# Optimization experiments

Measured on AMD Instinct MI355X. Metric: run time of the kernel, lower is better.

## Reference

```python
import jax, jax.numpy as jnp
import numpy as np
from functools import partial

C = 96
D_STATE = 16
D_CONV = 4
EXPAND = 2
D_INNER = EXPAND * C
DT_RANK = (C + 15) // 16  # ceil(96/16) = 6
EPS = 1e-6


def _ln_cf(x, w, b):
    # channels_first LayerNorm over axis=1 of [B,C,D,H,W]
    u = jnp.mean(x, axis=1, keepdims=True)
    s = jnp.mean((x - u) ** 2, axis=1, keepdims=True)
    xn = (x - u) / jnp.sqrt(s + EPS)
    return w[None, :, None, None, None] * xn + b[None, :, None, None, None]


def _ln_last(x, w, b):
    u = jnp.mean(x, axis=-1, keepdims=True)
    s = jnp.mean((x - u) ** 2, axis=-1, keepdims=True)
    return (x - u) / jnp.sqrt(s + 1e-5) * w + b


def _mamba(x, Win, conv_w, conv_b, Wx, Wdt, bdt, A_log, Dp, Wout):
    # x: [B, L, C]
    B, L, _ = x.shape
    xz = jnp.einsum('blc,ec->ble', x, Win)           # [B,L,2*di]
    xin, z = xz[..., :D_INNER], xz[..., D_INNER:]
    # depthwise causal conv along L
    xt = jnp.transpose(xin, (0, 2, 1))               # [B,di,L]
    xt = jnp.pad(xt, ((0, 0), (0, 0), (D_CONV - 1, 0)))
    xc = jax.lax.conv_general_dilated(
        xt, conv_w[:, None, :], window_strides=(1,), padding='VALID',
        feature_group_count=D_INNER, dimension_numbers=('NCH', 'OIH', 'NCH'))
    xc = jax.nn.silu(xc + conv_b[None, :, None])
    xc = jnp.transpose(xc, (0, 2, 1))                # [B,L,di]
    x_dbl = jnp.einsum('bld,ed->ble', xc, Wx)        # [B,L,dt_rank+2*ds]
    dt_r = x_dbl[..., :DT_RANK]
    Bm = x_dbl[..., DT_RANK:DT_RANK + D_STATE]       # [B,L,ds]
    Cm = x_dbl[..., DT_RANK + D_STATE:]              # [B,L,ds]
    dt = jax.nn.softplus(jnp.einsum('blr,dr->bld', dt_r, Wdt) + bdt)
    A = -jnp.exp(A_log)                              # [di,ds]
    dA = jnp.exp(dt[..., None] * A)                  # [B,L,di,ds]
    dBx = (dt * xc)[..., None] * Bm[:, :, None, :]   # [B,L,di,ds]

    def comb(e1, e2):
        a1, b1 = e1
        a2, b2 = e2
        return a1 * a2, a2 * b1 + b2

    _, h = jax.lax.associative_scan(comb, (dA, dBx), axis=1)
    y = jnp.einsum('blds,bls->bld', h, Cm) + xc * Dp
    y = y * jax.nn.silu(z)
    return jnp.einsum('bld,cd->blc', y, Wout)


def setup_inputs() -> dict:
    key = jax.random.key(0)
    ks = jax.random.split(key, 16)
    g = lambda k, sh: jax.random.normal(k, sh, dtype=jnp.float32) * 0.02
    inp = {
        'x': jax.random.normal(ks[0], (2, C, 20, 20, 20), dtype=jnp.float32),
        'ln_w': jnp.ones((C,), jnp.float32), 'ln_b': jnp.zeros((C,), jnp.float32),
        'mln_w': jnp.ones((C,), jnp.float32), 'mln_b': jnp.zeros((C,), jnp.float32),
        'Win': g(ks[1], (2 * D_INNER, C)),
        'conv_w': g(ks[2], (D_INNER, D_CONV)), 'conv_b': jnp.zeros((D_INNER,), jnp.float32),
        'Wx': g(ks[3], (DT_RANK + 2 * D_STATE, D_INNER)),
        'Wdt': g(ks[4], (D_INNER, DT_RANK)), 'bdt': g(ks[5], (D_INNER,)),
        'A_log': jnp.log(jnp.broadcast_to(jnp.arange(1, D_STATE + 1, dtype=jnp.float32), (D_INNER, D_STATE))),
        'Dp': jnp.ones((D_INNER,), jnp.float32),
        'Wout': g(ks[6], (C, D_INNER)),
        'proj_w': g(ks[7], (C, 3 * C)), 'proj_b': jnp.zeros((C,), jnp.float32),
        'fc1_w': g(ks[8], (4 * C, C)), 'fc1_b': jnp.zeros((4 * C,), jnp.float32),
        'fc2_w': g(ks[9], (C, 4 * C)), 'fc2_b': jnp.zeros((C,), jnp.float32),
    }
    return inp


def reference(x, ln_w, ln_b, mln_w, mln_b, Win, conv_w, conv_b, Wx, Wdt, bdt,
              A_log, Dp, Wout, proj_w, proj_b, fc1_w, fc1_b, fc2_w, fc2_b):
    B, Cc, Dd, Hh, Ww = x.shape
    L = Dd * Hh * Ww
    x1 = _ln_cf(x, ln_w, ln_b)
    # three directional flattenings (cube, so reshape shapes match)
    outs = []
    for perm in ((0, 1, 2, 3, 4), (0, 1, 3, 4, 2), (0, 1, 4, 2, 3)):
        xp = jnp.transpose(x1, perm)                     # [B,C,a,b,c]
        xf = jnp.transpose(xp.reshape(B, Cc, L), (0, 2, 1))  # [B,L,C]
        xf = _ln_last(xf, mln_w, mln_b)
        y = _mamba(xf, Win, conv_w, conv_b, Wx, Wdt, bdt, A_log, Dp, Wout)
        outs.append(jnp.transpose(y, (0, 2, 1)).reshape(B, Cc, Dd, Hh, Ww))
    cat = jnp.concatenate(outs, axis=1)                  # [B,3C,D,H,W]
    out1 = jnp.einsum('oc,bcdhw->bodhw', proj_w, cat) + proj_b[None, :, None, None, None]
    out_res = x + out1
    h = _ln_cf(out_res, ln_w, ln_b)
    h = jnp.einsum('oc,bcdhw->bodhw', fc1_w, h) + fc1_b[None, :, None, None, None]
    h = jax.nn.gelu(h, approximate=False)
    h = jnp.einsum('oc,bcdhw->bodhw', fc2_w, h) + fc2_b[None, :, None, None, None]
    return h + out_res
```

## Files before the change

kernel.cpp:

```cpp
#include <hip/hip_runtime.h>
#include <math.h>

#define S   8000
#define BB  2
#define CC  96
#define DI  192
#define NS  16
#define RK  6
#define GG  6
#define NC  200
#define LC  40
#define ND  38

typedef __attribute__((ext_vector_type(8))) short bf16x8;
typedef __attribute__((ext_vector_type(4))) float f32x4;
typedef __attribute__((ext_vector_type(2))) float f32x2;

__device__ __forceinline__ int pos_from_l(int dir, int l) {
  if (dir == 0) return l;
  int a  = l / 400;
  int r  = l - a * 400;
  int bq = r / 20;
  int cq = r - bq * 20;
  if (dir == 1) return cq * 400 + a * 20 + bq;
  return bq * 400 + cq * 20 + a;
}

__device__ __forceinline__ float silu(float z) {
  return z / (1.f + __expf(-z));
}

__device__ __forceinline__ unsigned short f2bf(float x) {
  unsigned int u = __float_as_uint(x);
  u += 0x7FFFu + ((u >> 16) & 1u);
  return (unsigned short)(u >> 16);
}

__device__ __forceinline__ float pair_sum(float y) {
  return y + __int_as_float(__builtin_amdgcn_update_dpp(
      0, __float_as_int(y), 0xB1, 0xF, 0xF, true));
}

__global__ __launch_bounds__(256) void k_ln2(const float* __restrict__ x,
    const float* __restrict__ lnw, const float* __restrict__ lnb,
    const float* __restrict__ mlnw, const float* __restrict__ mlnb,
    float* __restrict__ xn) {
  int t = blockIdx.x * blockDim.x + threadIdx.x;
  if (t >= BB * S) return;
  int b = t / S, pos = t - b * S;
  const float* xp = x + (size_t)b * CC * S + pos;
  float s1 = 0.f, s2 = 0.f;
  for (int c = 0; c < CC; ++c) { float v = xp[(size_t)c * S]; s1 += v; s2 += v * v; }
  float u = s1 * (1.f / CC);
  float var = s2 * (1.f / CC) - u * u;
  float rstd = rsqrtf(var + 1e-6f);
  float t1 = 0.f, t2 = 0.f;
  for (int c = 0; c < CC; ++c) {
    float y1 = fmaf(lnw[c], (xp[(size_t)c * S] - u) * rstd, lnb[c]);
    t1 += y1; t2 += y1 * y1;
  }
  float u2 = t1 * (1.f / CC);
  float var2 = t2 * (1.f / CC) - u2 * u2;
  float rstd2 = rsqrtf(var2 + 1e-5f);
  float* o = xn + (size_t)t * CC;
  for (int c = 0; c < CC; ++c) {
    float y1 = fmaf(lnw[c], (xp[(size_t)c * S] - u) * rstd, lnb[c]);
    o[c] = fmaf(mlnw[c], (y1 - u2) * rstd2, mlnb[c]);
  }
}

__global__ __launch_bounds__(256) void k_ln1(const float* __restrict__ xi,
    const float* __restrict__ lnw, const float* __restrict__ lnb,
    float* __restrict__ out) {
  int t = blockIdx.x * blockDim.x + threadIdx.x;
  if (t >= BB * S) return;
  int b = t / S, pos = t - b * S;
  const float* xp = xi + (size_t)b * CC * S + pos;
  float s1 = 0.f, s2 = 0.f;
  for (int c = 0; c < CC; ++c) { float v = xp[(size_t)c * S]; s1 += v; s2 += v * v; }
  float u = s1 * (1.f / CC);
  float var = s2 * (1.f / CC) - u * u;
  float rstd = rsqrtf(var + 1e-6f);
  float* o = out + (size_t)t * CC;
  for (int c = 0; c < CC; ++c)
    o[c] = fmaf(lnw[c], (xp[(size_t)c * S] - u) * rstd, lnb[c]);
}

#define BKP 40
template <int ACT, bool BIAS, bool RESID, bool OUT_BCS, bool GATEA>
__global__ __launch_bounds__(256) void k_mfma(const float* __restrict__ A,
    const float* __restrict__ Bw, const float* __restrict__ bias,
    const float* __restrict__ resid, const float* __restrict__ XZg,
    float* __restrict__ Cmat, int M, int N, int K) {
  __shared__ unsigned short Al[64][BKP];
  __shared__ unsigned short Bl[96][BKP];
  int tid = threadIdx.x;
  int m0 = blockIdx.x * 64, n0 = blockIdx.y * 96;
  int wid = tid >> 6, lane = tid & 63;
  int wr = wid >> 1, wc = wid & 1;
  int l16 = lane & 15, lk = (lane >> 4) * 8;
  f32x4 acc[2][3];
#pragma unroll
  for (int i = 0; i < 2; ++i)
#pragma unroll
    for (int j = 0; j < 3; ++j) acc[i][j] = (f32x4){0.f, 0.f, 0.f, 0.f};

  for (int kk = 0; kk < K; kk += 32) {
#pragma unroll
    for (int i = 0; i < 2; ++i) {
      int idx = tid + i * 256;
      int row = idx >> 3, kq = idx & 7;
      int m = m0 + row;
      float4 v = *(const float4*)&A[(size_t)m * K + kk + kq * 4];
      if (GATEA) {
        int bb = m / S, ll = m - bb * S;
        int j = kk + kq * 4;
        int dir = j / DI; int e0 = j - dir * DI;
        int p = pos_from_l(dir, ll);
        const float4 z4 = *(const float4*)&XZg[((size_t)bb * S + p) * 384 + DI + e0];
        v.x *= silu(z4.x); v.y *= silu(z4.y);
        v.z *= silu(z4.z); v.w *= silu(z4.w);
      }
      unsigned short* dst = &Al[row][kq * 4];
      dst[0] = f2bf(v.x); dst[1] = f2bf(v.y);
      dst[2] = f2bf(v.z); dst[3] = f2bf(v.w);
    }
#pragma unroll
    for (int i = 0; i < 3; ++i) {
      int idx = tid + i * 256;
      int bn = idx >> 3, kq = idx & 7;
      int n = n0 + bn;
      float4 v = make_float4(0.f, 0.f, 0.f, 0.f);
      if (n < N) v = *(const float4*)&Bw[(size_t)n * K + kk + kq * 4];
      unsigned short* dst = &Bl[bn][kq * 4];
      dst[0] = f2bf(v.x); dst[1] = f2bf(v.y);
      dst[2] = f2bf(v.z); dst[3] = f2bf(v.w);
    }
    __syncthreads();
    bf16x8 af[2], bfr[3];
#pragma unroll
    for (int i = 0; i < 2; ++i)
      af[i] = *(const bf16x8*)&Al[wr * 32 + i * 16 + l16][lk];
#pragma unroll
    for (int j = 0; j < 3; ++j)
      bfr[j] = *(const bf16x8*)&Bl[wc * 48 + j * 16 + l16][lk];
#pragma unroll
    for (int i = 0; i < 2; ++i)
#pragma unroll
      for (int j = 0; j < 3; ++j)
        acc[i][j] = __builtin_amdgcn_mfma_f32_16x16x32_bf16(
            af[i], bfr[j], acc[i][j], 0, 0, 0);
    __syncthreads();
  }
#pragma unroll
  for (int i = 0; i < 2; ++i) {
#pragma unroll
    for (int j = 0; j < 3; ++j) {
#pragma unroll
      for (int v = 0; v < 4; ++v) {
        int m = m0 + wr * 32 + i * 16 + (lane >> 4) * 4 + v;
        int n = n0 + wc * 48 + j * 16 + l16;
        if (n < N) {
          float val = acc[i][j][v];
          if (BIAS) val += bias[n];
          if (ACT == 1) val = 0.5f * val * (1.f + erff(val * 0.70710678118654752f));
          if (RESID || OUT_BCS) {
            int bb = m / S, pp = m - bb * S;
            size_t oidx = ((size_t)bb * CC + n) * S + pp;
            if (RESID) val += resid[oidx];
            if (OUT_BCS) { Cmat[oidx] = val; continue; }
          }
          Cmat[(size_t)m * N + n] = val;
        }
      }
    }
  }
}

__global__ __launch_bounds__(256) void k_conv(const float* __restrict__ XZ,
    const float* __restrict__ cw, const float* __restrict__ cb,
    float* __restrict__ xc) {
  int t = blockIdx.x * blockDim.x + threadIdx.x;
  if (t >= GG * S * 48) return;
  int q = t % 48; int gl = t / 48; int l = gl % S; int g = gl / S;
  int e0 = q * 4;
  int b = g / 3, dir = g - (g / 3) * 3;
  float cwv[4][4];
#pragma unroll
  for (int i = 0; i < 4; ++i)
    *(float4*)cwv[i] = *(const float4*)&cw[(e0 + i) * 4];
  float4 acc = *(const float4*)&cb[e0];
#pragma unroll
  for (int k = 0; k < 4; ++k) {
    int ls = l + k - 3;
    if (ls >= 0) {
      int p = pos_from_l(dir, ls);
      const float4 xz = *(const float4*)&XZ[((size_t)b * S + p) * 384 + e0];
      acc.x = fmaf(cwv[0][k], xz.x, acc.x);
      acc.y = fmaf(cwv[1][k], xz.y, acc.y);
      acc.z = fmaf(cwv[2][k], xz.z, acc.z);
      acc.w = fmaf(cwv[3][k], xz.w, acc.w);
    }
  }
  acc.x *= 1.f / (1.f + __expf(-acc.x));
  acc.y *= 1.f / (1.f + __expf(-acc.y));
  acc.z *= 1.f / (1.f + __expf(-acc.z));
  acc.w *= 1.f / (1.f + __expf(-acc.w));
  *(float4*)&xc[(size_t)gl * DI + e0] = acc;
}

__device__ __forceinline__ void stage_bc(float (*sBC)[40],
    const float* __restrict__ xdbl, int g, int c, int tid) {
  const float* src = xdbl + ((size_t)g * S + c * LC) * ND;
  for (int i = tid; i < LC * ND; i += 192) {
    int row = i / ND, col = i - row * ND;
    int dst = (col < RK) ? col : col + 2;
    sBC[row][dst] = src[(size_t)row * ND + col];
  }
}

#define DT_COMMON(l)                                                     \
  float a = bde;                                                         \
  {                                                                      \
    float4 r0 = *(const float4*)&sBC[l][0];                              \
    float2 r1 = *(const float2*)&sBC[l][4];                              \
    a = fmaf(wdt[0], r0.x, a); a = fmaf(wdt[1], r0.y, a);                \
    a = fmaf(wdt[2], r0.z, a); a = fmaf(wdt[3], r0.w, a);                \
    a = fmaf(wdt[4], r1.x, a); a = fmaf(wdt[5], r1.y, a);                \
  }                                                                      \
  float d = fmaxf(a, 0.f) + __logf(1.f + __expf(-fabsf(a)));

__global__ __launch_bounds__(192) void k_scanA(const float* __restrict__ xc,
    const float* __restrict__ xdbl, const float* __restrict__ Wdt,
    const float* __restrict__ bdt, const float* __restrict__ A_log,
    float* __restrict__ PA, float* __restrict__ EA) {
  __shared__ float sBC[LC][40];
  int c = blockIdx.x, g = blockIdx.y;
  int tid = threadIdx.x;
  int e = blockIdx.z * 96 + (tid >> 1);
  int hf = tid & 1;
  stage_bc(sBC, xdbl, g, c, tid);
  float wdt[RK];
#pragma unroll
  for (int r = 0; r < RK; ++r) wdt[r] = Wdt[e * RK + r];
  float bde = bdt[e];
  float base = -__expf(A_log[e * NS]);
  bool fast = true;
#pragma unroll
  for (int s = 1; s < NS; ++s) {
    float aes = -__expf(A_log[e * NS + s]);
    fast = fast && (fabsf(aes / base - (float)(s + 1)) < 1e-3f);
  }
  f32x2 h2[4];
#pragma unroll
  for (int k = 0; k < 4; ++k) h2[k] = (f32x2){0.f, 0.f};
  float T = 0.f;
  const float* xptr = xc + ((size_t)g * S + c * LC) * DI + e;
  __syncthreads();
  if (fast) {
    for (int l0 = 0; l0 < LC; l0 += 8) {
      float xb[8];
#pragma unroll
      for (int j = 0; j < 8; ++j) xb[j] = xptr[(size_t)(l0 + j) * DI];
#pragma unroll
      for (int j = 0; j < 8; ++j) {
        int l = l0 + j;
        DT_COMMON(l)
        T += d;
        float w = d * xb[j];
        float r = __expf(d * base);
        float r2 = r * r, r4 = r2 * r2, r8 = r4 * r4;
        float f = hf ? r8 * r : r;
        f32x2 m0 = {f, f * r};
        f32x2 r2v = {r2, r2};
        f32x2 r4v = {r4, r4};
        f32x2 m1 = m0 * r2v, m2 = m0 * r4v, m3 = m1 * r4v;
        f32x2 wv = {w, w};
        float4 Ba = *(const float4*)&sBC[l][8 + hf * 8];
        float4 Bb = *(const float4*)&sBC[l][12 + hf * 8];
        h2[0] = m0 * h2[0] + wv * (f32x2){Ba.x, Ba.y};
        h2[1] = m1 * h2[1] + wv * (f32x2){Ba.z, Ba.w};
        h2[2] = m2 * h2[2] + wv * (f32x2){Bb.x, Bb.y};
        h2[3] = m3 * h2[3] + wv * (f32x2){Bb.z, Bb.w};
      }
    }
  } else {
    float Aes[8];
#pragma unroll
    for (int k = 0; k < 8; ++k) Aes[k] = -__expf(A_log[e * NS + hf * 8 + k]);
#pragma unroll 1
    for (int l = 0; l < LC; ++l) {
      DT_COMMON(l)
      T += d;
      float w = d * xptr[(size_t)l * DI];
#pragma unroll
      for (int k = 0; k < 8; ++k) {
        float q = __expf(d * Aes[k]);
        h2[k >> 1][k & 1] = fmaf(q, h2[k >> 1][k & 1], w * sBC[l][8 + hf * 8 + k]);
      }
    }
  }
  float* pp = PA + (((size_t)g * NC + c) * DI + e) * NS + hf * 8;
  float* ep = EA + (((size_t)g * NC + c) * DI + e) * NS + hf * 8;
  float po[8];
  if (fast) {
    float r = __expf(base * T);
    float r2 = r * r, r4 = r2 * r2, r8 = r4 * r4;
    float f = hf ? r8 * r : r;
    po[0] = f; po[1] = f * r; po[2] = f * r2; po[3] = po[1] * r2;
    po[4] = f * r4; po[5] = po[1] * r4; po[6] = po[2] * r4; po[7] = po[3] * r4;
  } else {
#pragma unroll
    for (int k = 0; k < 8; ++k)
      po[k] = __expf(-__expf(A_log[e * NS + hf * 8 + k]) * T);
  }
  *(float4*)&pp[0] = make_float4(po[0], po[1], po[2], po[3]);
  *(float4*)&pp[4] = make_float4(po[4], po[5], po[6], po[7]);
  *(float4*)&ep[0] = make_float4(h2[0][0], h2[0][1], h2[1][0], h2[1][1]);
  *(float4*)&ep[4] = make_float4(h2[2][0], h2[2][1], h2[3][0], h2[3][1]);
}

__global__ __launch_bounds__(256) void k_scanB(const float* PA,
    const float* EA, float* Hin) {
  int idx = blockIdx.x * blockDim.x + threadIdx.x;
  if (idx >= GG * DI * NS) return;
  int g = idx / (DI * NS); int es = idx - g * (DI * NS);
  size_t stride = (size_t)DI * NS;
  size_t b0 = (size_t)g * NC * stride + es;
  float h = 0.f;
  for (int c0 = 0; c0 < NC; c0 += 8) {
    float p8[8], e8[8];
#pragma unroll
    for (int j = 0; j < 8; ++j) {
      size_t ix = b0 + (size_t)(c0 + j) * stride;
      p8[j] = PA[ix]; e8[j] = EA[ix];
    }
#pragma unroll
    for (int j = 0; j < 8; ++j) {
      size_t ix = b0 + (size_t)(c0 + j) * stride;
      Hin[ix] = h;
      h = fmaf(p8[j], h, e8[j]);
    }
  }
}

__global__ __launch_bounds__(192) void k_scanC(const float* __restrict__ xc,
    const float* __restrict__ xdbl, const float* __restrict__ Wdt,
    const float* __restrict__ bdt, const float* __restrict__ A_log,
    const float* __restrict__ Hin, const float* __restrict__ Dp,
    float* __restrict__ yg) {
  __shared__ float sBC[LC][40];
  int c = blockIdx.x, g = blockIdx.y;
  int tid = threadIdx.x;
  int e = blockIdx.z * 96 + (tid >> 1);
  int hf = tid & 1;
  const float* hp = Hin + (((size_t)g * NC + c) * DI + e) * NS + hf * 8;
  float4 h0 = *(const float4*)(hp + 0);
  float4 h1v = *(const float4*)(hp + 4);
  stage_bc(sBC, xdbl, g, c, tid);
  float wdt[RK];
#pragma unroll
  for (int r = 0; r < RK; ++r) wdt[r] = Wdt[e * RK + r];
  float bde = bdt[e];
  float dpe = Dp[e];
  float base = -__expf(A_log[e * NS]);
  bool fast = true;
#pragma unroll
  for (int s = 1; s < NS; ++s) {
    float aes = -__expf(A_log[e * NS + s]);
    fast = fast && (fabsf(aes / base - (float)(s + 1)) < 1e-3f);
  }
  f32x2 h2[4] = {{h0.x, h0.y}, {h0.z, h0.w}, {h1v.x, h1v.y}, {h1v.z, h1v.w}};
  const float* xptr = xc + ((size_t)g * S + c * LC) * DI + e;
  int b = g / 3, dir = g - (g / 3) * 3;
  float* yo = yg + ((size_t)b * S + c * LC) * 576 + dir * DI + e;
  __syncthreads();
  if (fast) {
    for (int l0 = 0; l0 < LC; l0 += 8) {
      float xb[8];
#pragma unroll
      for (int j = 0; j < 8; ++j) xb[j] = xptr[(size_t)(l0 + j) * DI];
#pragma unroll
      for (int j = 0; j < 8; ++j) {
        int l = l0 + j;
        DT_COMMON(l)
        float xv = xb[j];
        float w = d * xv;
        float r = __expf(d * base);
        float r2 = r * r, r4 = r2 * r2, r8 = r4 * r4;
        float f = hf ? r8 * r : r;
        f32x2 m0 = {f, f * r};
        f32x2 r2v = {r2, r2};
        f32x2 r4v = {r4, r4};
        f32x2 m1 = m0 * r2v, m2 = m0 * r4v, m3 = m1 * r4v;
        f32x2 wv = {w, w};
        float4 Ba = *(const float4*)&sBC[l][8 + hf * 8];
        float4 Bb = *(const float4*)&sBC[l][12 + hf * 8];
        float4 Ca = *(const float4*)&sBC[l][24 + hf * 8];
        float4 Cb = *(const float4*)&sBC[l][28 + hf * 8];
        f32x2 yacc = {hf ? 0.f : xv * dpe, 0.f};
        h2[0] = m0 * h2[0] + wv * (f32x2){Ba.x, Ba.y};
        yacc += h2[0] * (f32x2){Ca.x, Ca.y};
        h2[1] = m1 * h2[1] + wv * (f32x2){Ba.z, Ba.w};
        yacc += h2[1] * (f32x2){Ca.z, Ca.w};
        h2[2] = m2 * h2[2] + wv * (f32x2){Bb.x, Bb.y};
        yacc += h2[2] * (f32x2){Cb.x, Cb.y};
        h2[3] = m3 * h2[3] + wv * (f32x2){Bb.z, Bb.w};
        yacc += h2[3] * (f32x2){Cb.z, Cb.w};
        float ysum = pair_sum(yacc[0] + yacc[1]);
        if (!hf) yo[(size_t)l * 576] = ysum;
      }
    }
  } else {
    float Aes[8];
#pragma unroll
    for (int k = 0; k < 8; ++k) Aes[k] = -__expf(A_log[e * NS + hf * 8 + k]);
#pragma unroll 1
    for (int l = 0; l < LC; ++l) {
      DT_COMMON(l)
      float xv = xptr[(size_t)l * DI];
      float w = d * xv;
      float y = hf ? 0.f : xv * dpe;
#pragma unroll
      for (int k = 0; k < 8; ++k) {
        float q = __expf(d * Aes[k]);
        float hk = fmaf(q, h2[k >> 1][k & 1], w * sBC[l][8 + hf * 8 + k]);
        h2[k >> 1][k & 1] = hk;
        y = fmaf(hk, sBC[l][24 + hf * 8 + k], y);
      }
      float ysum = pair_sum(y);
      if (!hf) yo[(size_t)l * 576] = ysum;
    }
  }
}

__global__ __launch_bounds__(256) void k_foldW(const float* __restrict__ proj_w,
    const float* __restrict__ Wout, float* __restrict__ Mcat) {
  int t = blockIdx.x * blockDim.x + threadIdx.x;
  if (t >= CC * 576) return;
  int o = t / 576; int j = t - o * 576; int dir = j / DI; int e = j - dir * DI;
  float a = 0.f;
  for (int c2 = 0; c2 < CC; ++c2)
    a = fmaf(proj_w[o * 288 + dir * CC + c2], Wout[c2 * DI + e], a);
  Mcat[t] = a;
}

extern "C" void kernel_launch(void* const* d_in, const int* in_sizes, int n_in,
                              void* d_out, int out_size, void* d_ws, size_t ws_size,
                              hipStream_t stream) {
  const float* x      = (const float*)d_in[0];
  const float* ln_w   = (const float*)d_in[1];
  const float* ln_b   = (const float*)d_in[2];
  const float* mln_w  = (const float*)d_in[3];
  const float* mln_b  = (const float*)d_in[4];
  const float* Win    = (const float*)d_in[5];
  const float* conv_w = (const float*)d_in[6];
  const float* conv_b = (const float*)d_in[7];
  const float* Wx     = (const float*)d_in[8];
  const float* Wdt    = (const float*)d_in[9];
  const float* bdt    = (const float*)d_in[10];
  const float* A_log  = (const float*)d_in[11];
  const float* Dp     = (const float*)d_in[12];
  const float* Wout   = (const float*)d_in[13];
  const float* proj_w = (const float*)d_in[14];
  const float* proj_b = (const float*)d_in[15];
  const float* fc1_w  = (const float*)d_in[16];
  const float* fc1_b  = (const float*)d_in[17];
  const float* fc2_w  = (const float*)d_in[18];
  const float* fc2_b  = (const float*)d_in[19];

  float* ws = (float*)d_ws;
  size_t off = 0;
  float* xn   = ws + off; off += (size_t)BB * S * CC;
  float* XZ   = ws + off; off += (size_t)BB * S * 384;
  float* xc   = ws + off; off += (size_t)GG * S * DI;
  float* xdbl = ws + off; off += (size_t)GG * S * ND;
  float* PA   = ws + off; off += (size_t)GG * NC * DI * NS;
  float* EA   = ws + off; off += (size_t)GG * NC * DI * NS;
  float* yg   = ws + off; off += (size_t)BB * S * 576;
  float* Mcat = ws + off; off += (size_t)CC * 576;
  if (ws_size < off * sizeof(float)) return;
  float* Hin  = PA;
  float* ores = xn;
  float* xln2 = xc;
  float* h1   = XZ;

  k_ln2<<<(BB * S + 255) / 256, 256, 0, stream>>>(x, ln_w, ln_b, mln_w, mln_b, xn);
  k_mfma<0, false, false, false, false>
      <<<dim3(BB * S / 64, 4), 256, 0, stream>>>(
      xn, Win, nullptr, nullptr, nullptr, XZ, BB * S, 384, CC);
  k_conv<<<(GG * S * 48 + 255) / 256, 256, 0, stream>>>(XZ, conv_w, conv_b, xc);
  k_mfma<0, false, false, false, false>
      <<<dim3(GG * S / 64, 1), 256, 0, stream>>>(
      xc, Wx, nullptr, nullptr, nullptr, xdbl, GG * S, ND, DI);
  k_scanA<<<dim3(NC, GG, 2), 192, 0, stream>>>(xc, xdbl, Wdt, bdt, A_log, PA, EA);
  k_scanB<<<(GG * DI * NS + 255) / 256, 256, 0, stream>>>(PA, EA, Hin);
  k_scanC<<<dim3(NC, GG, 2), 192, 0, stream>>>(xc, xdbl, Wdt, bdt, A_log, Hin, Dp, yg);
  k_foldW<<<(CC * 576 + 255) / 256, 256, 0, stream>>>(proj_w, Wout, Mcat);
  k_mfma<0, true, true, true, true>
      <<<dim3(BB * S / 64, 1), 256, 0, stream>>>(
      yg, Mcat, proj_b, x, XZ, ores, BB * S, CC, 576);
  k_ln1<<<(BB * S + 255) / 256, 256, 0, stream>>>(ores, ln_w, ln_b, xln2);
  k_mfma<1, true, false, false, false>
      <<<dim3(BB * S / 64, 4), 256, 0, stream>>>(
      xln2, fc1_w, fc1_b, nullptr, nullptr, h1, BB * S, 384, CC);
  k_mfma<0, true, true, true, false>
      <<<dim3(BB * S / 64, 1), 256, 0, stream>>>(
      h1, fc2_w, fc2_b, ores, nullptr, (float*)d_out, BB * S, CC, 384);
}
```

Before: 283.1 us.

## Fuse LayerNorms into following GEMMs and store intermediates as bf16

```diff
diff --git a/kernel.cpp b/kernel.cpp
--- a/kernel.cpp
+++ b/kernel.cpp
@@ -35,60 +35,130 @@
   u += 0x7FFFu + ((u >> 16) & 1u);
   return (unsigned short)(u >> 16);
 }
+__device__ __forceinline__ float bf2f(unsigned short h) {
+  return __uint_as_float((unsigned int)h << 16);
+}
 
 __device__ __forceinline__ float pair_sum(float y) {
   return y + __int_as_float(__builtin_amdgcn_update_dpp(
       0, __float_as_int(y), 0xB1, 0xF, 0xF, true));
 }
-
-__global__ __launch_bounds__(256) void k_ln2(const float* __restrict__ x,
+__device__ __forceinline__ float quad_sum(float x) {
+  x += __int_as_float(__builtin_amdgcn_update_dpp(0, __float_as_int(x), 0xB1, 0xF, 0xF, true));
+  x += __int_as_float(__builtin_amdgcn_update_dpp(0, __float_as_int(x), 0x4E, 0xF, 0xF, true));
+  return x;
+}
+
+template <int ACT, bool DOUBLE, bool OUTBF16>
+__global__ __launch_bounds__(256) void k_lnmfma(const float* __restrict__ Xsrc,
     const float* __restrict__ lnw, const float* __restrict__ lnb,
     const float* __restrict__ mlnw, const float* __restrict__ mlnb,
-    float* __restrict__ xn) {
-  int t = blockIdx.x * blockDim.x + threadIdx.x;
-  if (t >= BB * S) return;
-  int b = t / S, pos = t - b * S;
-  const float* xp = x + (size_t)b * CC * S + pos;
-  float s1 = 0.f, s2 = 0.f;
-  for (int c = 0; c < CC; ++c) { float v = xp[(size_t)c * S]; s1 += v; s2 += v * v; }
-  float u = s1 * (1.f / CC);
-  float var = s2 * (1.f / CC) - u * u;
-  float rstd = rsqrtf(var + 1e-6f);
-  float t1 = 0.f, t2 = 0.f;
-  for (int c = 0; c < CC; ++c) {
-    float y1 = fmaf(lnw[c], (xp[(size_t)c * S] - u) * rstd, lnb[c]);
-    t1 += y1; t2 += y1 * y1;
-  }
-  float u2 = t1 * (1.f / CC);
-  float var2 = t2 * (1.f / CC) - u2 * u2;
-  float rstd2 = rsqrtf(var2 + 1e-5f);
-  float* o = xn + (size_t)t * CC;
-  for (int c = 0; c < CC; ++c) {
-    float y1 = fmaf(lnw[c], (xp[(size_t)c * S] - u) * rstd, lnb[c]);
-    o[c] = fmaf(mlnw[c], (y1 - u2) * rstd2, mlnb[c]);
-  }
-}
-
-__global__ __launch_bounds__(256) void k_ln1(const float* __restrict__ xi,
-    const float* __restrict__ lnw, const float* __restrict__ lnb,
-    float* __restrict__ out) {
-  int t = blockIdx.x * blockDim.x + threadIdx.x;
-  if (t >= BB * S) return;
-  int b = t / S, pos = t - b * S;
-  const float* xp = xi + (size_t)b * CC * S + pos;
-  float s1 = 0.f, s2 = 0.f;
-  for (int c = 0; c < CC; ++c) { float v = xp[(size_t)c * S]; s1 += v; s2 += v * v; }
-  float u = s1 * (1.f / CC);
-  float var = s2 * (1.f / CC) - u * u;
-  float rstd = rsqrtf(var + 1e-6f);
-  float* o = out + (size_t)t * CC;
-  for (int c = 0; c < CC; ++c)
-    o[c] = fmaf(lnw[c], (xp[(size_t)c * S] - u) * rstd, lnb[c]);
+    const float* __restrict__ Bw, const float* __restrict__ bias,
+    void* __restrict__ Cout, int M, int N) {
+  __shared__ float Xf[64][97];
+  __shared__ unsigned short Al[64][104];
+  __shared__ unsigned short Bl[96][104];
+  int tid = threadIdx.x;
+  int m0 = blockIdx.x * 64, n0 = blockIdx.y * 96;
+  int b = m0 / S, pos0 = m0 - b * S;
+  for (int idx = tid; idx < 64 * 96; idx += 256) {
+    int row = idx & 63, c = idx >> 6;
+    Xf[row][c] = Xsrc[((size_t)b * CC + c) * S + pos0 + row];
+  }
+  for (int idx = tid; idx < 96 * 24; idx += 256) {
+    int bn = idx / 24, kq = idx - bn * 24;
+    int n = n0 + bn;
+    float4 v = make_float4(0.f, 0.f, 0.f, 0.f);
+    if (n < N) v = *(const float4*)&Bw[(size_t)n * 96 + kq * 4];
+    unsigned short* dst = &Bl[bn][kq * 4];
+    dst[0] = f2bf(v.x); dst[1] = f2bf(v.y);
+    dst[2] = f2bf(v.z); dst[3] = f2bf(v.w);
+  }
+  __syncthreads();
+  {
+    int row = tid >> 2, part = tid & 3;
+    const float* xr = &Xf[row][part * 24];
+    float s1 = 0.f, s2 = 0.f;
+#pragma unroll
+    for (int i = 0; i < 24; ++i) { float v = xr[i]; s1 += v; s2 += v * v; }
+    s1 = quad_sum(s1); s2 = quad_sum(s2);
+    float u = s1 * (1.f / 96.f);
+    float var = s2 * (1.f / 96.f) - u * u;
+    float rstd = rsqrtf(var + 1e-6f);
+    if (DOUBLE) {
+      float t1 = 0.f, t2 = 0.f;
+#pragma unroll
+      for (int i = 0; i < 24; ++i) {
+        int c = part * 24 + i;
+        float y1 = fmaf(lnw[c], (xr[i] - u) * rstd, lnb[c]);
+        t1 += y1; t2 += y1 * y1;
+      }
+      t1 = quad_sum(t1); t2 = quad_sum(t2);
+      float u2 = t1 * (1.f / 96.f);
+      float var2 = t2 * (1.f / 96.f) - u2 * u2;
+      float rstd2 = rsqrtf(var2 + 1e-5f);
+#pragma unroll
+      for (int i = 0; i < 24; ++i) {
+        int c = part * 24 + i;
+        float y1 = fmaf(lnw[c], (xr[i] - u) * rstd, lnb[c]);
+        Al[row][c] = f2bf(fmaf(mlnw[c], (y1 - u2) * rstd2, mlnb[c]));
+      }
+    } else {
+#pragma unroll
+      for (int i = 0; i < 24; ++i) {
+        int c = part * 24 + i;
+        Al[row][c] = f2bf(fmaf(lnw[c], (xr[i] - u) * rstd, lnb[c]));
+      }
+    }
+  }
+  __syncthreads();
+  int wid = tid >> 6, lane = tid & 63;
+  int wr = wid >> 1, wc = wid & 1;
+  int l16 = lane & 15, lk = (lane >> 4) * 8;
+  f32x4 acc[2][3];
+#pragma unroll
+  for (int i = 0; i < 2; ++i)
+#pragma unroll
+    for (int j = 0; j < 3; ++j) acc[i][j] = (f32x4){0.f, 0.f, 0.f, 0.f};
+#pragma unroll
+  for (int kc = 0; kc < 96; kc += 32) {
+    bf16x8 af[2], bfr[3];
+#pragma unroll
+    for (int i = 0; i < 2; ++i)
+      af[i] = *(const bf16x8*)&Al[wr * 32 + i * 16 + l16][kc + lk];
+#pragma unroll
+    for (int j = 0; j < 3; ++j)
+      bfr[j] = *(const bf16x8*)&Bl[wc * 48 + j * 16 + l16][kc + lk];
+#pragma unroll
+    for (int i = 0; i < 2; ++i)
+#pragma unroll
+      for (int j = 0; j < 3; ++j)
+        acc[i][j] = __builtin_amdgcn_mfma_f32_16x16x32_bf16(
+            af[i], bfr[j], acc[i][j], 0, 0, 0);
+  }
+#pragma unroll
+  for (int i = 0; i < 2; ++i) {
+#pragma unroll
+    for (int j = 0; j < 3; ++j) {
+#pragma unroll
+      for (int v = 0; v < 4; ++v) {
+        int m = m0 + wr * 32 + i * 16 + (lane >> 4) * 4 + v;
+        int n = n0 + wc * 48 + j * 16 + l16;
+        if (n < N) {
+          float val = acc[i][j][v];
+          val += bias ? bias[n] : 0.f;
+          if (ACT == 1) val = 0.5f * val * (1.f + erff(val * 0.70710678118654752f));
+          if (OUTBF16) ((unsigned short*)Cout)[(size_t)m * N + n] = f2bf(val);
+          else         ((float*)Cout)[(size_t)m * N + n] = val;
+        }
+      }
+    }
+  }
 }
 
 #define BKP 40
-template <int ACT, bool BIAS, bool RESID, bool OUT_BCS, bool GATEA>
-__global__ __launch_bounds__(256) void k_mfma(const float* __restrict__ A,
+template <int ACT, bool BIAS, bool RESID, bool OUT_BCS, bool GATEA, bool ABF16>
+__global__ __launch_bounds__(256) void k_mfma(const void* __restrict__ Ap,
     const float* __restrict__ Bw, const float* __restrict__ bias,
     const float* __restrict__ resid, const float* __restrict__ XZg,
     float* __restrict__ Cmat, int M, int N, int K) {
@@ -106,24 +176,41 @@
     for (int j = 0; j < 3; ++j) acc[i][j] = (f32x4){0.f, 0.f, 0.f, 0.f};
 
   for (int kk = 0; kk < K; kk += 32) {
-#pragma unroll
-    for (int i = 0; i < 2; ++i) {
-      int idx = tid + i * 256;
-      int row = idx >> 3, kq = idx & 7;
+    if (ABF16) {
+      int row = tid >> 2, kq = tid & 3;
       int m = m0 + row;
-      float4 v = *(const float4*)&A[(size_t)m * K + kk + kq * 4];
+      const unsigned short* As = (const unsigned short*)Ap;
+      uint4 v = *(const uint4*)&As[(size_t)m * K + kk + kq * 8];
       if (GATEA) {
+        unsigned short* pv = (unsigned short*)&v;
         int bb = m / S, ll = m - bb * S;
-        int j = kk + kq * 4;
+        int j = kk + kq * 8;
         int dir = j / DI; int e0 = j - dir * DI;
         int p = pos_from_l(dir, ll);
-        const float4 z4 = *(const float4*)&XZg[((size_t)bb * S + p) * 384 + DI + e0];
-        v.x *= silu(z4.x); v.y *= silu(z4.y);
-        v.z *= silu(z4.z); v.w *= silu(z4.w);
-      }
-      unsigned short* dst = &Al[row][kq * 4];
-      dst[0] = f2bf(v.x); dst[1] = f2bf(v.y);
-      dst[2] = f2bf(v.z); dst[3] = f2bf(v.w);
+        const float4 z1 = *(const float4*)&XZg[((size_t)bb * S + p) * 384 + DI + e0];
+        const float4 z2 = *(const float4*)&XZg[((size_t)bb * S + p) * 384 + DI + e0 + 4];
+        pv[0] = f2bf(bf2f(pv[0]) * silu(z1.x));
+        pv[1] = f2bf(bf2f(pv[1]) * silu(z1.y));
+        pv[2] = f2bf(bf2f(pv[2]) * silu(z1.z));
+        pv[3] = f2bf(bf2f(pv[3]) * silu(z1.w));
+        pv[4] = f2bf(bf2f(pv[4]) * silu(z2.x));
+        pv[5] = f2bf(bf2f(pv[5]) * silu(z2.y));
+        pv[6] = f2bf(bf2f(pv[6]) * silu(z2.z));
+        pv[7] = f2bf(bf2f(pv[7]) * silu(z2.w));
+      }
+      *(uint4*)&Al[row][kq * 8] = v;
+    } else {
+#pragma unroll
+      for (int i = 0; i < 2; ++i) {
+        int idx = tid + i * 256;
+        int row = idx >> 3, kq = idx & 7;
+        int m = m0 + row;
+        const float* Af = (const float*)Ap;
+        float4 v = *(const float4*)&Af[(size_t)m * K + kk + kq * 4];
+        unsigned short* dst = &Al[row][kq * 4];
+        dst[0] = f2bf(v.x); dst[1] = f2bf(v.y);
+        dst[2] = f2bf(v.z); dst[3] = f2bf(v.w);
+      }
     }
 #pragma unroll
     for (int i = 0; i < 3; ++i) {
@@ -348,7 +435,7 @@
     const float* __restrict__ xdbl, const float* __restrict__ Wdt,
     const float* __restrict__ bdt, const float* __restrict__ A_log,
     const float* __restrict__ Hin, const float* __restrict__ Dp,
-    float* __restrict__ yg) {
+    unsigned short* __restrict__ ygb) {
   __shared__ float sBC[LC][40];
   int c = blockIdx.x, g = blockIdx.y;
   int tid = threadIdx.x;
@@ -373,7 +460,7 @@
   f32x2 h2[4] = {{h0.x, h0.y}, {h0.z, h0.w}, {h1v.x, h1v.y}, {h1v.z, h1v.w}};
   const float* xptr = xc + ((size_t)g * S + c * LC) * DI + e;
   int b = g / 3, dir = g - (g / 3) * 3;
-  float* yo = yg + ((size_t)b * S + c * LC) * 576 + dir * DI + e;
+  unsigned short* yo = ygb + ((size_t)b * S + c * LC) * 576 + dir * DI + e;
   __syncthreads();
   if (fast) {
     for (int l0 = 0; l0 < LC; l0 += 8) {
@@ -408,7 +495,7 @@
         h2[3] = m3 * h2[3] + wv * (f32x2){Bb.z, Bb.w};
         yacc += h2[3] * (f32x2){Cb.z, Cb.w};
         float ysum = pair_sum(yacc[0] + yacc[1]);
-        if (!hf) yo[(size_t)l * 576] = ysum;
+        if (!hf) yo[(size_t)l * 576] = f2bf(ysum);
       }
     }
   } else {
@@ -429,7 +516,7 @@
         y = fmaf(hk, sBC[l][24 + hf * 8 + k], y);
       }
       float ysum = pair_sum(y);
-      if (!hf) yo[(size_t)l * 576] = ysum;
+      if (!hf) yo[(size_t)l * 576] = f2bf(ysum);
     }
   }
 }
@@ -471,7 +558,7 @@
 
   float* ws = (float*)d_ws;
   size_t off = 0;
-  float* xn   = ws + off; off += (size_t)BB * S * CC;
+  float* ores = ws + off; off += (size_t)BB * S * CC;
   float* XZ   = ws + off; off += (size_t)BB * S * 384;
   float* xc   = ws + off; off += (size_t)GG * S * DI;
   float* xdbl = ws + off; off += (size_t)GG * S * ND;
@@ -481,30 +568,25 @@
   float* Mcat = ws + off; off += (size_t)CC * 576;
   if (ws_size < off * sizeof(float)) return;
   float* Hin  = PA;
-  float* ores = xn;
-  float* xln2 = xc;
-  float* h1   = XZ;
-
-  k_ln2<<<(BB * S + 255) / 256, 256, 0, stream>>>(x, ln_w, ln_b, mln_w, mln_b, xn);
-  k_mfma<0, false, false, false, false>
-      <<<dim3(BB * S / 64, 4), 256, 0, stream>>>(
-      xn, Win, nullptr, nullptr, nullptr, XZ, BB * S, 384, CC);
+  unsigned short* ygb = (unsigned short*)yg;
+  unsigned short* h1  = (unsigned short*)XZ;
+
+  k_lnmfma<0, true, false><<<dim3(BB * S / 64, 4), 256, 0, stream>>>(
+      x, ln_w, ln_b, mln_w, mln_b, Win, nullptr, XZ, BB * S, 384);
   k_conv<<<(GG * S * 48 + 255) / 256, 256, 0, stream>>>(XZ, conv_w, conv_b, xc);
-  k_mfma<0, false, false, false, false>
+  k_mfma<0, false, false, false, false, false>
       <<<dim3(GG * S / 64, 1), 256, 0, stream>>>(
       xc, Wx, nullptr, nullptr, nullptr, xdbl, GG * S, ND, DI);
   k_scanA<<<dim3(NC, GG, 2), 192, 0, stream>>>(xc, xdbl, Wdt, bdt, A_log, PA, EA);
   k_scanB<<<(GG * DI * NS + 255) / 256, 256, 0, stream>>>(PA, EA, Hin);
-  k_scanC<<<dim3(NC, GG, 2), 192, 0, stream>>>(xc, xdbl, Wdt, bdt, A_log, Hin, Dp, yg);
+  k_scanC<<<dim3(NC, GG, 2), 192, 0, stream>>>(xc, xdbl, Wdt, bdt, A_log, Hin, Dp, ygb);
   k_foldW<<<(CC * 576 + 255) / 256, 256, 0, stream>>>(proj_w, Wout, Mcat);
-  k_mfma<0, true, true, true, true>
+  k_mfma<0, true, true, true, true, true>
       <<<dim3(BB * S / 64, 1), 256, 0, stream>>>(
-      yg, Mcat, proj_b, x, XZ, ores, BB * S, CC, 576);
-  k_ln1<<<(BB * S + 255) / 256, 256, 0, stream>>>(ores, ln_w, ln_b, xln2);
-  k_mfma<1, true, false, false, false>
-      <<<dim3(BB * S / 64, 4), 256, 0, stream>>>(
-      xln2, fc1_w, fc1_b, nullptr, nullptr, h1, BB * S, 384, CC);
-  k_mfma<0, true, true, true, false>
+      ygb, Mcat, proj_b, x, XZ, ores, BB * S, CC, 576);
+  k_lnmfma<1, false, true><<<dim3(BB * S / 64, 4), 256, 0, stream>>>(
+      ores, ln_w, ln_b, nullptr, nullptr, fc1_w, fc1_b, h1, BB * S, 384);
+  k_mfma<0, true, true, true, false, true>
       <<<dim3(BB * S / 64, 1), 256, 0, stream>>>(
       h1, fc2_w, fc2_b, ores, nullptr, (float*)d_out, BB * S, CC, 384);
 }
```

Measured after the change: 267.9 us. 5.4% less time.
